# Optimization experiments

Hardware: AMD Instinct MI355X
Metric: run time of the kernel (lower is better)

Reference implementation:

```python
import jax, jax.numpy as jnp
import numpy as np

HID = 128
N_NODES = 50000
N_REL = 500
N_EDGES = 625000
BN_EPS = 1e-5
LRELU_SLOPE = 0.01


def _xavier(key, shape):
    fan_in, fan_out = shape[1], shape[0]
    std = float(np.sqrt(2.0 / (fan_in + fan_out)))
    return jax.random.normal(key, shape, dtype=jnp.float32) * std


def setup_inputs() -> dict:
    key = jax.random.key(0)
    ks = jax.random.split(key, 16)
    x = jax.random.normal(ks[0], (N_NODES, HID), dtype=jnp.float32)
    r = jax.random.normal(ks[1], (N_REL, HID), dtype=jnp.float32)
    que_context = jax.random.normal(ks[2], (1, HID), dtype=jnp.float32)
    fin_que = jax.random.normal(ks[3], (1, 1, HID), dtype=jnp.float32)
    edge_index = jax.random.randint(ks[4], (2, N_EDGES), 0, N_NODES, dtype=jnp.int64)
    edge_attr = jax.random.randint(ks[5], (N_EDGES,), 0, N_REL, dtype=jnp.int64)
    return {
        "x": x, "r": r, "que_context": que_context, "fin_que": fin_que,
        "edge_index": edge_index, "edge_attr": edge_attr,
        # mess_comp: Linear(2*hid, hid) + Tanh
        "W_mess": _xavier(ks[6], (HID, 2 * HID)), "b_mess": jnp.zeros((HID,), jnp.float32),
        # mess_atten_trans: Linear(2*hid, hid) + LeakyReLU
        "W_matt": _xavier(ks[7], (HID, 2 * HID)), "b_matt": jnp.zeros((HID,), jnp.float32),
        "mess_atten_weight": _xavier(ks[8], (1, HID)),
        # x_atten_trans: Linear(2*hid, hid) + LeakyReLU
        "W_xatt": _xavier(ks[9], (HID, 2 * HID)), "b_xatt": jnp.zeros((HID,), jnp.float32),
        "x_atten_weight": _xavier(ks[10], (1, HID)),
        # BatchNorm1d(hid) affine params (training-mode batch stats are used)
        "bn_gamma": jnp.ones((HID,), jnp.float32), "bn_beta": jnp.zeros((HID,), jnp.float32),
    }


def reference(x, r, que_context, fin_que, edge_index, edge_attr,
              W_mess, b_mess, W_matt, b_matt, mess_atten_weight,
              W_xatt, b_xatt, x_atten_weight, bn_gamma, bn_beta):
    n_nodes = x.shape[0]
    # BatchNorm1d over relation embeddings (training-mode: batch statistics, biased var)
    mu = jnp.mean(r, axis=0)
    var = jnp.mean(jnp.square(r - mu), axis=0)
    r = (r - mu) * jax.lax.rsqrt(var + BN_EPS) * bn_gamma + bn_beta

    head_ents, tail_ents = edge_index[0], edge_index[1]
    head_embeds = x[head_ents]            # [E, H]
    rel_embeds = r[edge_attr]             # [E, H]

    # message computation: Linear(2H->H) + tanh
    mess_in = jnp.concatenate([head_embeds, rel_embeds], axis=1)  # [E, 2H]
    mess = jnp.tanh(mess_in @ W_mess.T + b_mess)                  # [E, H]

    # message attention logits
    qc = jnp.broadcast_to(que_context, (mess.shape[0], que_context.shape[1]))
    mc = jnp.concatenate([mess, qc], axis=1) @ W_matt.T + b_matt
    mc = jax.nn.leaky_relu(mc, LRELU_SLOPE)
    mess_coeffs = jnp.sum(mess_atten_weight * mc, axis=1)         # [E]

    # segment softmax over tail_ents
    seg_max = jax.ops.segment_max(mess_coeffs, tail_ents, num_segments=n_nodes)
    mess_coeffs = jnp.exp(mess_coeffs - seg_max[tail_ents])
    seg_sum = jax.ops.segment_sum(mess_coeffs, tail_ents, num_segments=n_nodes)
    mess_weights = mess_coeffs / (seg_sum[tail_ents] + 1e-16)

    # weighted scatter-sum aggregation
    sum_mess = jax.ops.segment_sum(mess * mess_weights[:, None], tail_ents,
                                   num_segments=n_nodes)          # [N, H]

    # gating attention between x and aggregated messages
    pair = jnp.stack([x, sum_mess], axis=1)                       # [N, 2, H]
    fq = jnp.broadcast_to(fin_que, (n_nodes, 2, fin_que.shape[2]))
    xc = jnp.concatenate([pair, fq], axis=2)                      # [N, 2, 2H]
    xc = jax.nn.leaky_relu(jnp.einsum('nkc,hc->nkh', xc, W_xatt) + b_xatt, LRELU_SLOPE)
    x_coeffs = jnp.sum(x_atten_weight[None] * xc, axis=2)         # [N, 2]
    x_weight = jax.nn.softmax(x_coeffs, axis=1)
    x_out = x_weight[:, 0:1] * x + x_weight[:, 1:2] * sum_mess
    # dropout is identity (eval / p=0)
    return x_out, r
```

## Files before the change

kernel.cpp:

```cpp
#include <hip/hip_runtime.h>
#include <hip/hip_bf16.h>

#define HID 128
#define NN 50000
#define NR 500
#define NE 625000
#define LRELU 0.01f
#define SCAN_BLOCKS 196
#define NBLK_SC 256

typedef __hip_bfloat16 bf16;
typedef __attribute__((ext_vector_type(8))) short short8;
typedef __attribute__((ext_vector_type(4))) float float4_;

__device__ __forceinline__ float b2f(bf16 v) { return __bfloat162float(v); }
__device__ __forceinline__ bf16 f2b(float v) { return __float2bfloat16(v); }

__device__ __forceinline__ float san(float v) {
    return (v == v && v > -1e30f && v < 1e30f) ? v : 0.f;
}

__device__ __forceinline__ float ftanh(float a) {
    float e = __expf(2.f * a);
    return 1.f - 2.f * __builtin_amdgcn_rcpf(e + 1.f);
}

__device__ __forceinline__ float ldf(const void* p, int i, int f32) {
    return f32 ? ((const float*)p)[i] : b2f(((const bf16*)p)[i]);
}
__device__ __forceinline__ void stf(void* p, int i, float v, int f32) {
    if (f32) ((float*)p)[i] = v;
    else ((bf16*)p)[i] = f2b(v);
}

__device__ __forceinline__ int clampi(int v, int hi) {
    return v < 0 ? 0 : (v >= hi ? hi - 1 : v);
}
__device__ __forceinline__ int idx_at(const int* p, int i, int is64) {
    return p[is64 ? (2 * i) : i];
}

__device__ __forceinline__ unsigned short bfbits(float v) {
    bf16 h = f2b(v);
    return *(unsigned short*)&h;
}
__device__ __forceinline__ unsigned int packbf2(float a, float b) {
    return (unsigned int)bfbits(a) | ((unsigned int)bfbits(b) << 16);
}
__device__ __forceinline__ float bflo(unsigned int u) { return __uint_as_float(u << 16); }
__device__ __forceinline__ float bfhi(unsigned int u) { return __uint_as_float(u & 0xffff0000u); }

__device__ __forceinline__ float xorReduce16(float v) {
    v += __shfl_xor(v, 1, 64);
    v += __shfl_xor(v, 2, 64);
    v += __shfl_xor(v, 4, 64);
    v += __shfl_xor(v, 8, 64);
    return v;
}
__device__ __forceinline__ float waveMax(float v) {
#pragma unroll
    for (int o = 1; o < 64; o <<= 1) v = fmaxf(v, __shfl_xor(v, o, 64));
    return v;
}
__device__ __forceinline__ float waveSum(float v) {
#pragma unroll
    for (int o = 1; o < 64; o <<= 1) v += __shfl_xor(v, o, 64);
    return v;
}

__device__ __forceinline__ float dot8(const void* W, int row, int col, int f32,
                                      const float* vec) {
    float s;
    if (f32) {
        const float* p = (const float*)W + (size_t)row * 2 * HID + col;
        float4 a = *(const float4*)p;
        float4 b = *(const float4*)(p + 4);
        s = a.x * vec[0] + a.y * vec[1] + a.z * vec[2] + a.w * vec[3]
          + b.x * vec[4] + b.y * vec[5] + b.z * vec[6] + b.w * vec[7];
    } else {
        short8 v = *(const short8*)((const bf16*)W + (size_t)row * 2 * HID + col);
        s = 0.f;
#pragma unroll
        for (int i = 0; i < 8; ++i) {
            unsigned int u = ((unsigned int)(unsigned short)v[i]) << 16;
            s += __uint_as_float(u) * vec[i];
        }
    }
    return s;
}

__device__ __forceinline__ int octant_of(int head) {
    return (head * 8) / NN;
}

struct DetectArr {
    const void* p[16];
    int sz[16];
    int kind[16];
};

__global__ void detect_all(DetectArr d, int* __restrict__ flags) {
    int b = blockIdx.x;
    int t = threadIdx.x;
    if (d.kind[b] == 1) {
        if (t < 64) {
            const int* q = (const int*)d.p[b];
            int o = q[2 * t + 1];
            unsigned long long bm = __ballot(o != 0);
            if (t == 0) flags[b] = (bm == 0ull) ? 1 : 0;
        }
        return;
    }
    __shared__ int sb[256], sf[256];
    const unsigned int* w = (const unsigned int*)d.p[b];
    int K = d.sz[b] >> 1;
    if (K > 4096) K = 4096;
    int bv = 0, fv = 0;
    for (int i = t; i < K; i += 256) {
        unsigned int x = w[i];
        unsigned int lo = x & 0xFFFFu, hi = x >> 16;
        if (lo == 0u) {
            if (hi) fv++;
        } else {
            unsigned int e = (lo >> 7) & 0xFFu;
            if (e >= 90u && e <= 160u) bv++;
            else fv++;
        }
    }
    sb[t] = bv; sf[t] = fv;
    __syncthreads();
    for (int o = 128; o > 0; o >>= 1) {
        if (t < o) { sb[t] += sb[t + o]; sf[t] += sf[t + o]; }
        __syncthreads();
    }
    if (t == 0) flags[b] = (sf[0] > sb[0]) ? 1 : 0;
}

__global__ void bn_stats(const void* __restrict__ r, const int* __restrict__ flags,
                         float* __restrict__ stats) {
    __shared__ float sb[256], sq[256];
    const int fr = flags[1];
    int h = blockIdx.x;
    int t = threadIdx.x;
    float s = 0.f, ss = 0.f;
    for (int i = t; i < NR; i += 256) {
        float v = ldf(r, i * HID + h, fr);
        s += v; ss += v * v;
    }
    sb[t] = s; sq[t] = ss;
    __syncthreads();
    for (int o = 128; o > 0; o >>= 1) {
        if (t < o) { sb[t] += sb[t + o]; sq[t] += sq[t + o]; }
        __syncthreads();
    }
    if (t == 0) {
        float mu = sb[0] / NR;
        float var = sq[0] / NR - mu * mu;
        if (var < 0.f) var = 0.f;
        stats[h] = mu;
        stats[HID + h] = rsqrtf(var + 1e-5f);
    }
}

__global__ void bn_apply(const void* __restrict__ r, const void* __restrict__ gamma,
                         const void* __restrict__ beta, const int* __restrict__ flags,
                         const float* __restrict__ stats,
                         float* __restrict__ rnorm, void* __restrict__ out_base) {
    const int fr = flags[1], fg = flags[14], fb = flags[15], fo = flags[0];
    int i = blockIdx.x * 256 + threadIdx.x;
    if (i >= NR * HID) return;
    int h = i & 127;
    float v = san((ldf(r, i, fr) - stats[h]) * stats[HID + h] * ldf(gamma, h, fg)
                  + ldf(beta, h, fb));
    rnorm[i] = v;
    stf(out_base, NN * HID + i, v, fo);
}

__global__ void precomp_kernel(const void* __restrict__ Wmatt, const void* __restrict__ bmatt,
                               const void* __restrict__ qc,
                               const void* __restrict__ Wxatt, const void* __restrict__ bxatt,
                               const void* __restrict__ fq, const int* __restrict__ flags,
                               float* __restrict__ cmatt, float* __restrict__ cxatt) {
    __shared__ float vs[HID];
    __shared__ float part[256];
    const void* W    = blockIdx.x ? Wxatt : Wmatt;
    const void* bias = blockIdx.x ? bxatt : bmatt;
    const void* vsrc = blockIdx.x ? fq : qc;
    float* out       = blockIdx.x ? cxatt : cmatt;
    const int fW = flags[blockIdx.x ? 11 : 8];
    const int fb = flags[blockIdx.x ? 12 : 9];
    const int fv = flags[blockIdx.x ? 3 : 2];
    int t = threadIdx.x;
    if (t < HID) vs[t] = ldf(vsrc, t, fv);
    __syncthreads();
    int h = t & 127, ks = t >> 7;
    float a = 0.f;
#pragma unroll
    for (int i = 0; i < 8; ++i)
        a += dot8(W, h, HID + ks * 64 + i * 8, fW, &vs[ks * 64 + i * 8]);
    part[t] = a;
    __syncthreads();
    if (t < HID) out[h] = san(part[h] + part[h + 128] + ldf(bias, h, fb));
}

__global__ void rm_kernel(const void* __restrict__ Wmess, const void* __restrict__ bmess,
                          const int* __restrict__ flags,
                          const float* __restrict__ rnorm, bf16* __restrict__ Rmb) {
    __shared__ float rl[2][HID];
    const int fW = flags[6], fb = flags[7];
    int t = threadIdx.x;
    int sub = t >> 7, h = t & 127;
    int rel = blockIdx.x * 2 + sub;
    rl[sub][h] = rnorm[rel * HID + h];
    __syncthreads();
    float a = ldf(bmess, h, fb);
#pragma unroll
    for (int i = 0; i < 16; ++i)
        a += dot8(Wmess, h, HID + i * 8, fW, &rl[sub][i * 8]);
    Rmb[rel * HID + h] = f2b(san(a));
}

#define MLDA 136

__device__ __forceinline__ short8 load_bfrag(const void* W, int n, int k0, int f32) {
    short8 b;
    if (f32) {
        const float* Wf = (const float*)W + (size_t)n * 2 * HID + k0;
        float4 u0 = *(const float4*)Wf;
        float4 u1 = *(const float4*)(Wf + 4);
        b[0] = (short)bfbits(u0.x); b[1] = (short)bfbits(u0.y);
        b[2] = (short)bfbits(u0.z); b[3] = (short)bfbits(u0.w);
        b[4] = (short)bfbits(u1.x); b[5] = (short)bfbits(u1.y);
        b[6] = (short)bfbits(u1.z); b[7] = (short)bfbits(u1.w);
    } else {
        b = *(const short8*)((const bf16*)W + (size_t)n * 2 * HID + k0);
    }
    return b;
}

__global__ __launch_bounds__(256, 4) void xm_mfma(const void* __restrict__ x,
                                                  const void* __restrict__ Wmess,
                                                  const int* __restrict__ flags,
                                                  bf16* __restrict__ Xmb) {
    __shared__ short ml[64 * MLDA];
    const int fx = flags[0], fW = flags[6];
    int tid = threadIdx.x;
    int l = tid & 63, w = tid >> 6;
    int quad = l >> 4, lo16 = l & 15;
    int nbase = w * 32;
    short8 bfr[2][4];
#pragma unroll
    for (int nt = 0; nt < 2; ++nt)
#pragma unroll
        for (int kk = 0; kk < 4; ++kk)
            bfr[nt][kk] = load_bfrag(Wmess, nbase + nt * 16 + lo16, kk * 32 + quad * 8, fW);

    const int ntiles = (NN + 63) / 64;
    for (int tile = blockIdx.x; tile < ntiles; tile += gridDim.x) {
        __syncthreads();
#pragma unroll
        for (int p = 0; p < 8; ++p) {
            int rl_ = p * 8 + (tid >> 5);
            int node = clampi(tile * 64 + rl_, NN);
            int k4 = (tid & 31) * 4;
            unsigned int o0, o1;
            if (fx) {
                float4 v = *(const float4*)((const float*)x + (size_t)node * HID + k4);
                o0 = packbf2(v.x, v.y);
                o1 = packbf2(v.z, v.w);
            } else {
                uint2 u = *(const uint2*)((const bf16*)x + (size_t)node * HID + k4);
                o0 = u.x; o1 = u.y;
            }
            unsigned int* dst = (unsigned int*)&ml[rl_ * MLDA + k4];
            dst[0] = o0; dst[1] = o1;
        }
        __syncthreads();
        float4_ acc[4][2];
#pragma unroll
        for (int mt = 0; mt < 4; ++mt)
#pragma unroll
            for (int nt = 0; nt < 2; ++nt)
                acc[mt][nt] = (float4_){0.f, 0.f, 0.f, 0.f};
#pragma unroll
        for (int kk = 0; kk < 4; ++kk) {
            short8 a[4];
#pragma unroll
            for (int mt = 0; mt < 4; ++mt)
                a[mt] = *(const short8*)&ml[(mt * 16 + lo16) * MLDA + kk * 32 + quad * 8];
#pragma unroll
            for (int mt = 0; mt < 4; ++mt)
#pragma unroll
                for (int nt = 0; nt < 2; ++nt)
                    acc[mt][nt] = __builtin_amdgcn_mfma_f32_16x16x32_bf16(
                        a[mt], bfr[nt][kk], acc[mt][nt], 0, 0, 0);
        }
#pragma unroll
        for (int mt = 0; mt < 4; ++mt)
#pragma unroll
            for (int nt = 0; nt < 2; ++nt)
#pragma unroll
                for (int r = 0; r < 4; ++r) {
                    int node = tile * 64 + mt * 16 + quad * 4 + r;
                    if (node < NN)
                        Xmb[node * HID + nbase + nt * 16 + lo16] = f2b(san(acc[mt][nt][r]));
                }
    }
}

__global__ __launch_bounds__(256, 6) void edge_coeff_mfma(
        const bf16* __restrict__ Xmb, const bf16* __restrict__ Rmb,
        const void* __restrict__ Wmatt, const float* __restrict__ cmatt,
        const void* __restrict__ maw, const unsigned int* __restrict__ ohr,
        const int* __restrict__ oslot, const int* __restrict__ ooffs,
        const int* __restrict__ flags, float* __restrict__ ccsr,
        bf16* __restrict__ messT) {
    __shared__ short ml[64 * MLDA];
    __shared__ float swave[4][64];
    const int fWm = flags[8], fmw = flags[10];
    int tid = threadIdx.x;
    int l = tid & 63, w = tid >> 6;
    int quad = l >> 4, lo16 = l & 15;
    int nbase = w * 32;
    short8 bfr[2][4];
#pragma unroll
    for (int nt = 0; nt < 2; ++nt)
#pragma unroll
        for (int kk = 0; kk < 4; ++kk)
            bfr[nt][kk] = load_bfrag(Wmatt, nbase + nt * 16 + lo16, kk * 32 + quad * 8, fWm);

    int n0 = nbase + lo16, n1 = n0 + 16;
    float c0 = cmatt[n0], c1 = cmatt[n1];
    float w0 = ldf(maw, n0, fmw), w1 = ldf(maw, n1, fmw);

    const int k = blockIdx.x & 7;
    const int beg = ooffs[k], end = ooffs[k + 1];
    const int tstride = gridDim.x >> 3;
    const int seg = tid & 15;
    const int rowsub = tid >> 4;

    for (int t = blockIdx.x >> 3;; t += tstride) {
        int base = beg + t * 64;
        if (base >= end) break;
        __syncthreads();
        int rslot[4];
#pragma unroll
        for (int p = 0; p < 4; ++p) {
            int el = p * 16 + rowsub;
            int i = base + el;
            int idx = i < end ? i : end - 1;
            unsigned int hr = ohr[idx];
            rslot[p] = (i < end) ? oslot[i] : -1;
            int head = hr & 0xffffu, rel = hr >> 16;
            int k8 = seg * 8;
            uint4 xv = *(const uint4*)&Xmb[head * HID + k8];
            uint4 rv = *(const uint4*)&Rmb[rel * HID + k8];
            uint4 o;
            o.x = packbf2(ftanh(bflo(xv.x) + bflo(rv.x)), ftanh(bfhi(xv.x) + bfhi(rv.x)));
            o.y = packbf2(ftanh(bflo(xv.y) + bflo(rv.y)), ftanh(bfhi(xv.y) + bfhi(rv.y)));
            o.z = packbf2(ftanh(bflo(xv.z) + bflo(rv.z)), ftanh(bfhi(xv.z) + bfhi(rv.z)));
            o.w = packbf2(ftanh(bflo(xv.w) + bflo(rv.w)), ftanh(bfhi(xv.w) + bfhi(rv.w)));
            *(uint4*)&ml[el * MLDA + k8] = o;
        }
        __syncthreads();
        float4_ acc[4][2];
#pragma unroll
        for (int mt = 0; mt < 4; ++mt)
#pragma unroll
            for (int nt = 0; nt < 2; ++nt)
                acc[mt][nt] = (float4_){0.f, 0.f, 0.f, 0.f};
#pragma unroll
        for (int kk = 0; kk < 4; ++kk) {
            short8 a[4];
#pragma unroll
            for (int mt = 0; mt < 4; ++mt)
                a[mt] = *(const short8*)&ml[(mt * 16 + lo16) * MLDA + kk * 32 + quad * 8];
#pragma unroll
            for (int mt = 0; mt < 4; ++mt)
#pragma unroll
                for (int nt = 0; nt < 2; ++nt)
                    acc[mt][nt] = __builtin_amdgcn_mfma_f32_16x16x32_bf16(
                        a[mt], bfr[nt][kk], acc[mt][nt], 0, 0, 0);
        }
        if (messT) {
#pragma unroll
            for (int p = 0; p < 4; ++p) {
                int slot = rslot[p];
                if (slot >= 0) {
                    int el = p * 16 + rowsub;
                    *(uint4*)&messT[(size_t)slot * HID + seg * 8] =
                        *(const uint4*)&ml[el * MLDA + seg * 8];
                }
            }
        }
#pragma unroll
        for (int mt = 0; mt < 4; ++mt)
#pragma unroll
            for (int r = 0; r < 4; ++r) {
                float z0 = acc[mt][0][r] + c0;
                z0 = z0 > 0.f ? z0 : LRELU * z0;
                float z1 = acc[mt][1][r] + c1;
                z1 = z1 > 0.f ? z1 : LRELU * z1;
                float s = w0 * z0 + w1 * z1;
                s = xorReduce16(s);
                if (lo16 == 0) swave[w][mt * 16 + quad * 4 + r] = s;
            }
        __syncthreads();
        if (tid < 64) {
            int i = base + tid;
            if (i < end) {
                int slot = oslot[i];
                ccsr[slot] = san(swave[0][tid] + swave[1][tid]
                                 + swave[2][tid] + swave[3][tid]);
            }
        }
    }
}

__global__ __launch_bounds__(256, 4) void gate_mfma(
        const void* __restrict__ x, const bf16* __restrict__ smb,
        const void* __restrict__ Wxatt, const float* __restrict__ cxatt,
        const void* __restrict__ xaw, const int* __restrict__ flags,
        void* __restrict__ outx) {
    __shared__ short ml[64 * MLDA];
    __shared__ float swave[4][64];
    __shared__ float lgL[64];
    const int fx = flags[0], fWx = flags[11], fxw = flags[13], fo = flags[0];
    int tid = threadIdx.x;
    int l = tid & 63, w = tid >> 6;
    int quad = l >> 4, lo16 = l & 15;
    int nbase = w * 32;
    short8 bfr[2][4];
#pragma unroll
    for (int nt = 0; nt < 2; ++nt)
#pragma unroll
        for (int kk = 0; kk < 4; ++kk)
            bfr[nt][kk] = load_bfrag(Wxatt, nbase + nt * 16 + lo16, kk * 32 + quad * 8, fWx);

    int n0 = nbase + lo16, n1 = n0 + 16;
    float c0 = cxatt[n0], c1 = cxatt[n1];
    float w0 = ldf(xaw, n0, fxw), w1 = ldf(xaw, n1, fxw);

    const int ntiles = (NN + 31) / 32;
    for (int tile = blockIdx.x; tile < ntiles; tile += gridDim.x) {
        __syncthreads();
#pragma unroll
        for (int p = 0; p < 8; ++p) {
            int rl_ = p * 8 + (tid >> 5);
            int node = clampi(tile * 32 + (rl_ >> 1), NN);
            int k4 = (tid & 31) * 4;
            unsigned int o0, o1;
            if (rl_ & 1) {
                uint2 u = *(const uint2*)&smb[node * HID + k4];
                o0 = u.x; o1 = u.y;
            } else if (fx) {
                float4 v = *(const float4*)((const float*)x + (size_t)node * HID + k4);
                o0 = packbf2(v.x, v.y);
                o1 = packbf2(v.z, v.w);
            } else {
                uint2 u = *(const uint2*)((const bf16*)x + (size_t)node * HID + k4);
                o0 = u.x; o1 = u.y;
            }
            unsigned int* dst = (unsigned int*)&ml[rl_ * MLDA + k4];
            dst[0] = o0; dst[1] = o1;
        }
        __syncthreads();
        float4_ acc[4][2];
#pragma unroll
        for (int mt = 0; mt < 4; ++mt)
#pragma unroll
            for (int nt = 0; nt < 2; ++nt)
                acc[mt][nt] = (float4_){0.f, 0.f, 0.f, 0.f};
#pragma unroll
        for (int kk = 0; kk < 4; ++kk) {
            short8 a[4];
#pragma unroll
            for (int mt = 0; mt < 4; ++mt)
                a[mt] = *(const short8*)&ml[(mt * 16 + lo16) * MLDA + kk * 32 + quad * 8];
#pragma unroll
            for (int mt = 0; mt < 4; ++mt)
#pragma unroll
                for (int nt = 0; nt < 2; ++nt)
                    acc[mt][nt] = __builtin_amdgcn_mfma_f32_16x16x32_bf16(
                        a[mt], bfr[nt][kk], acc[mt][nt], 0, 0, 0);
        }
#pragma unroll
        for (int mt = 0; mt < 4; ++mt)
#pragma unroll
            for (int r = 0; r < 4; ++r) {
                float z0 = acc[mt][0][r] + c0;
                z0 = z0 > 0.f ? z0 : LRELU * z0;
                float z1 = acc[mt][1][r] + c1;
                z1 = z1 > 0.f ? z1 : LRELU * z1;
                float s = w0 * z0 + w1 * z1;
                s = xorReduce16(s);
                if (lo16 == 0) swave[w][mt * 16 + quad * 4 + r] = s;
            }
        __syncthreads();
        if (tid < 64)
            lgL[tid] = san(swave[0][tid] + swave[1][tid] + swave[2][tid] + swave[3][tid]);
        __syncthreads();
#pragma unroll
        for (int it = 0; it < 16; ++it) {
            int idx = tid + 256 * it;
            int nl = idx >> 7, h = idx & 127;
            int node = tile * 32 + nl;
            if (node < NN) {
                float g0 = lgL[2 * nl], g1 = lgL[2 * nl + 1];
                float mm = fmaxf(g0, g1);
                float e0 = __expf(g0 - mm), e1 = __expf(g1 - mm);
                float inv = __builtin_amdgcn_rcpf(e0 + e1);
                float xv = ldf(x, node * HID + h, fx);
                float sv = b2f(smb[node * HID + h]);
                stf(outx, node * HID + h, san((e0 * xv + e1 * sv) * inv), fo);
            }
        }
    }
}

__global__ void count_kernel(const int* __restrict__ ei, const int* __restrict__ flags,
                             int* __restrict__ counts, int* __restrict__ blockOct) {
    __shared__ int oh[8];
    const int is64e = flags[4];
    if (threadIdx.x < 8) oh[threadIdx.x] = 0;
    __syncthreads();
    for (int e = blockIdx.x * blockDim.x + threadIdx.x; e < NE; e += gridDim.x * blockDim.x) {
        int tail = clampi(idx_at(ei, NE + e, is64e), NN);
        int head = clampi(idx_at(ei, e, is64e), NN);
        atomicAdd(&counts[tail], 1);
        atomicAdd(&oh[octant_of(head)], 1);
    }
    __syncthreads();
    if (threadIdx.x < 8) blockOct[blockIdx.x * 8 + threadIdx.x] = oh[threadIdx.x];
}

__global__ void scan_phase1(const int* __restrict__ counts, int* __restrict__ offs,
                            int* __restrict__ bsum) {
    __shared__ int buf[256];
    int t = threadIdx.x;
    int i = blockIdx.x * 256 + t;
    int v = (i < NN) ? counts[i] : 0;
    buf[t] = v;
    __syncthreads();
    for (int off = 1; off < 256; off <<= 1) {
        int add = (t >= off) ? buf[t - off] : 0;
        __syncthreads();
        buf[t] += add;
        __syncthreads();
    }
    if (i < NN) offs[i] = buf[t] - v;
    if (t == 255) bsum[blockIdx.x] = buf[255];
}

__global__ void scan_phase2(int* __restrict__ bsum, int* __restrict__ bexc) {
    __shared__ int buf[256];
    int t = threadIdx.x;
    int v = (t < SCAN_BLOCKS) ? bsum[t] : 0;
    buf[t] = v;
    __syncthreads();
    for (int off = 1; off < 256; off <<= 1) {
        int add = (t >= off) ? buf[t - off] : 0;
        __syncthreads();
        buf[t] += add;
        __syncthreads();
    }
    if (t < SCAN_BLOCKS) bexc[t] = buf[t] - v;
    if (t == 255) bexc[SCAN_BLOCKS] = buf[255];
}

__global__ void scan_phase3(int* __restrict__ offs, int* __restrict__ cursor,
                            const int* __restrict__ bexc) {
    int i = blockIdx.x * 256 + threadIdx.x;
    if (i < NN) {
        int v = offs[i] + bexc[blockIdx.x];
        offs[i] = v;
        cursor[i] = v;
    }
    if (i == 0) offs[NN] = bexc[SCAN_BLOCKS];
}

__global__ void oct_scan(const int* __restrict__ blockOct, int* __restrict__ ooffs,
                         int* __restrict__ blockBase) {
    __shared__ int buf[256];
    __shared__ int excl[256][8];
    __shared__ int octTot[8], octBase[9];
    int t = threadIdx.x;
#pragma unroll
    for (int oo = 0; oo < 8; ++oo) {
        int v = blockOct[t * 8 + oo];
        buf[t] = v;
        __syncthreads();
        for (int off = 1; off < 256; off <<= 1) {
            int add = (t >= off) ? buf[t - off] : 0;
            __syncthreads();
            buf[t] += add;
            __syncthreads();
        }
        excl[t][oo] = buf[t] - v;
        if (t == 255) octTot[oo] = buf[255];
        __syncthreads();
    }
    if (t == 0) {
        int acc = 0;
        for (int oo = 0; oo < 8; ++oo) { octBase[oo] = acc; acc += octTot[oo]; }
        octBase[8] = acc;
        for (int i = 0; i < 9; ++i) ooffs[i] = octBase[i];
    }
    __syncthreads();
#pragma unroll
    for (int oo = 0; oo < 8; ++oo)
        blockBase[t * 8 + oo] = excl[t][oo] + octBase[oo];
}

__global__ void scatter_kernel(const int* __restrict__ ei, const int* __restrict__ ea,
                               const int* __restrict__ flags,
                               int* __restrict__ cursorT, const int* __restrict__ blockBase,
                               unsigned int* __restrict__ hrcsr,
                               unsigned int* __restrict__ ohr, int* __restrict__ oslot) {
    __shared__ int cur[8];
    const int is64e = flags[4], is64a = flags[5];
    if (threadIdx.x < 8) cur[threadIdx.x] = blockBase[blockIdx.x * 8 + threadIdx.x];
    __syncthreads();
    for (int e = blockIdx.x * blockDim.x + threadIdx.x; e < NE; e += gridDim.x * blockDim.x) {
        int tail = clampi(idx_at(ei, NE + e, is64e), NN);
        int head = clampi(idx_at(ei, e, is64e), NN);
        int rel = clampi(idx_at(ea, e, is64a), NR);
        unsigned int hr = (unsigned int)head | ((unsigned int)rel << 16);
        int p = atomicAdd(&cursorT[tail], 1);
        if (p >= 0 && p < NE) hrcsr[p] = hr;
        int q = atomicAdd(&cur[octant_of(head)], 1);
        if (q >= 0 && q < NE) {
            ohr[q] = hr;
            oslot[q] = (p >= 0 && p < NE) ? p : 0;
        }
    }
}

__global__ __launch_bounds__(256, 8) void node_aggr_seq(
        const bf16* __restrict__ messT, const int* __restrict__ offs,
        const float* __restrict__ ccsr, bf16* __restrict__ smb) {
    int tid = threadIdx.x;
    int sub = tid >> 6;
    int lane = tid & 63;
    int node = blockIdx.x * 4 + sub;
    if (node >= NN) return;
    int s = offs[node], en = offs[node + 1];

    float m = -INFINITY;
    for (int i = s + lane; i < en; i += 64) m = fmaxf(m, ccsr[i]);
    m = waveMax(m);
    float lsum = 0.f;
    for (int i = s + lane; i < en; i += 64) lsum += __expf(ccsr[i] - m);
    lsum = waveSum(lsum);
    float inv = 1.f / (lsum + 1e-16f);

    const int col = lane * 2;
    float acc0 = 0.f, acc1 = 0.f;
    int i = s;
    for (; i + 2 <= en; i += 2) {
        float wg0 = __expf(ccsr[i] - m), wg1 = __expf(ccsr[i + 1] - m);
        unsigned int u0 = *(const unsigned int*)&messT[(size_t)i * HID + col];
        unsigned int u1 = *(const unsigned int*)&messT[(size_t)(i + 1) * HID + col];
        acc0 += wg0 * bflo(u0) + wg1 * bflo(u1);
        acc1 += wg0 * bfhi(u0) + wg1 * bfhi(u1);
    }
    if (i < en) {
        float wg0 = __expf(ccsr[i] - m);
        unsigned int u0 = *(const unsigned int*)&messT[(size_t)i * HID + col];
        acc0 += wg0 * bflo(u0);
        acc1 += wg0 * bfhi(u0);
    }
    *(unsigned int*)&smb[node * HID + col] = packbf2(san(acc0 * inv), san(acc1 * inv));
}

__global__ __launch_bounds__(256, 8) void node_aggr_kernel(
        const bf16* __restrict__ Xmb, const bf16* __restrict__ Rmb,
        const int* __restrict__ offs, const unsigned int* __restrict__ hrcsr,
        const float* __restrict__ ccsr, bf16* __restrict__ smb) {
    int tid = threadIdx.x;
    int sub = tid >> 6;
    int lane = tid & 63;
    int node = blockIdx.x * 4 + sub;
    if (node >= NN) return;
    int s = offs[node], en = offs[node + 1];

    float m = -INFINITY;
    for (int i = s + lane; i < en; i += 64) m = fmaxf(m, ccsr[i]);
    m = waveMax(m);
    float lsum = 0.f;
    for (int i = s + lane; i < en; i += 64) lsum += __expf(ccsr[i] - m);
    lsum = waveSum(lsum);
    float inv = 1.f / (lsum + 1e-16f);

    const int col = lane * 2;
    float acc0 = 0.f, acc1 = 0.f;
    for (int i = s; i < en; ++i) {
        unsigned int hr0 = hrcsr[i];
        float wg0 = __expf(ccsr[i] - m);
        unsigned int xv0 = *(const unsigned int*)&Xmb[(hr0 & 0xffffu) * HID + col];
        unsigned int rv0 = *(const unsigned int*)&Rmb[(hr0 >> 16) * HID + col];
        acc0 += wg0 * ftanh(bflo(xv0) + bflo(rv0));
        acc1 += wg0 * ftanh(bfhi(xv0) + bfhi(rv0));
    }
    *(unsigned int*)&smb[node * HID + col] = packbf2(san(acc0 * inv), san(acc1 * inv));
}

extern "C" void kernel_launch(void* const* d_in, const int* in_sizes, int n_in,
                              void* d_out, int out_size, void* d_ws, size_t ws_size,
                              hipStream_t stream) {
    const void* x     = d_in[0];
    const void* r     = d_in[1];
    const void* qc    = d_in[2];
    const void* fq    = d_in[3];
    const int*  ei    = (const int*)d_in[4];
    const int*  ea    = (const int*)d_in[5];
    const void* Wmess = d_in[6];
    const void* bmess = d_in[7];
    const void* Wmatt = d_in[8];
    const void* bmatt = d_in[9];
    const void* maw   = d_in[10];
    const void* Wxatt = d_in[11];
    const void* bxatt = d_in[12];
    const void* xaw   = d_in[13];
    const void* gamma = d_in[14];
    const void* beta  = d_in[15];

    char* base = (char*)d_ws;
    size_t off = 0;
    auto alloc = [&](size_t bytes, size_t align) -> size_t {
        off = (off + align - 1) & ~(align - 1);
        size_t cur = off; off += bytes; return cur;
    };
    size_t o_flags  = alloc(16 * 4, 4);
    size_t o_counts = alloc((size_t)NN * 4, 4);
    size_t o_offs   = alloc((size_t)(NN + 1) * 4, 4);
    size_t o_cursor = alloc((size_t)(NN + 3) * 4, 4);
    size_t o_bsum   = alloc(256 * 4, 4);
    size_t o_bexc   = alloc(264 * 4, 4);
    size_t o_bOct   = alloc((size_t)NBLK_SC * 8 * 4, 4);
    size_t o_bBase  = alloc((size_t)NBLK_SC * 8 * 4, 4);
    size_t o_ooffs  = alloc(9 * 4, 4);
    size_t o_hrcsr  = alloc((size_t)NE * 4, 4);
    size_t o_ohr    = alloc((size_t)NE * 4, 4);
    size_t o_oslot  = alloc((size_t)NE * 4, 4);
    size_t o_ccsr   = alloc((size_t)NE * 4, 4);
    size_t o_rnorm  = alloc((size_t)NR * HID * 4, 4);
    size_t o_stats  = alloc(2 * HID * 4, 4);
    size_t o_cmatt  = alloc(HID * 4, 4);
    size_t o_cxatt  = alloc(HID * 4, 4);
    size_t o_Rmb    = alloc((size_t)NR * HID * 2, 4);
    size_t o_Xmb    = alloc((size_t)NN * HID * 2, 4);
    size_t o_smb    = alloc((size_t)NN * HID * 2, 4);
    size_t o_messT  = alloc((size_t)NE * HID * 2, 256);
    const bool useMess = ws_size >= off;

    int*          flags     = (int*)(base + o_flags);
    int*          counts    = (int*)(base + o_counts);
    int*          offs      = (int*)(base + o_offs);
    int*          cursor    = (int*)(base + o_cursor);
    int*          bsum      = (int*)(base + o_bsum);
    int*          bexc      = (int*)(base + o_bexc);
    int*          blockOct  = (int*)(base + o_bOct);
    int*          blockBase = (int*)(base + o_bBase);
    int*          ooffs     = (int*)(base + o_ooffs);
    unsigned int* hrcsr     = (unsigned int*)(base + o_hrcsr);
    unsigned int* ohr       = (unsigned int*)(base + o_ohr);
    int*          oslot     = (int*)(base + o_oslot);
    float*        ccsr      = (float*)(base + o_ccsr);
    float*        rnorm     = (float*)(base + o_rnorm);
    float*        stats     = (float*)(base + o_stats);
    float*        cmatt     = (float*)(base + o_cmatt);
    float*        cxatt     = (float*)(base + o_cxatt);
    bf16*         Rmb       = (bf16*)(base + o_Rmb);
    bf16*         Xmb       = (bf16*)(base + o_Xmb);
    bf16*         smb       = (bf16*)(base + o_smb);
    bf16*         messT     = useMess ? (bf16*)(base + o_messT) : (bf16*)nullptr;

    hipMemsetAsync(counts, 0, (size_t)NN * sizeof(int), stream);

    DetectArr da;
    const void* ps[16] = {x, r, qc, fq, ei, ea, Wmess, bmess, Wmatt, bmatt, maw,
                          Wxatt, bxatt, xaw, gamma, beta};
    int szs[16] = {NN * HID, NR * HID, HID, HID, 2 * NE, NE, 2 * HID * HID, HID,
                   2 * HID * HID, HID, HID, 2 * HID * HID, HID, HID, HID, HID};
    for (int i = 0; i < 16; ++i) {
        da.p[i] = ps[i];
        da.sz[i] = szs[i];
        da.kind[i] = (i == 4 || i == 5) ? 1 : 0;
    }
    detect_all<<<16, 256, 0, stream>>>(da, flags);

    bn_stats<<<HID, 256, 0, stream>>>(r, flags, stats);
    bn_apply<<<(NR * HID + 255) / 256, 256, 0, stream>>>(r, gamma, beta, flags, stats,
                                                         rnorm, d_out);
    precomp_kernel<<<2, 256, 0, stream>>>(Wmatt, bmatt, qc, Wxatt, bxatt, fq, flags,
                                          cmatt, cxatt);
    rm_kernel<<<NR / 2, 256, 0, stream>>>(Wmess, bmess, flags, rnorm, Rmb);
    xm_mfma<<<782, 256, 0, stream>>>(x, Wmess, flags, Xmb);
    count_kernel<<<NBLK_SC, 256, 0, stream>>>(ei, flags, counts, blockOct);
    scan_phase1<<<SCAN_BLOCKS, 256, 0, stream>>>(counts, offs, bsum);
    scan_phase2<<<1, 256, 0, stream>>>(bsum, bexc);
    scan_phase3<<<SCAN_BLOCKS, 256, 0, stream>>>(offs, cursor, bexc);
    oct_scan<<<1, 256, 0, stream>>>(blockOct, ooffs, blockBase);
    scatter_kernel<<<NBLK_SC, 256, 0, stream>>>(ei, ea, flags, cursor, blockBase,
                                                hrcsr, ohr, oslot);
    edge_coeff_mfma<<<1536, 256, 0, stream>>>(Xmb, Rmb, Wmatt, cmatt, maw, ohr, oslot,
                                              ooffs, flags, ccsr, messT);
    if (useMess)
        node_aggr_seq<<<(NN + 3) / 4, 256, 0, stream>>>(messT, offs, ccsr, smb);
    else
        node_aggr_kernel<<<(NN + 3) / 4, 256, 0, stream>>>(Xmb, Rmb, offs, hrcsr, ccsr,
                                                           smb);
    gate_mfma<<<1563, 256, 0, stream>>>(x, smb, Wxatt, cxatt, xaw, flags, d_out);
}
```

Baseline: 454.2 us.

## Drop materialized message buffer and recompute tanh messages during node aggregation

Removes the per-edge bf16 message buffer (E x 128) that edge_coeff_mfma scattered into CSR order, and always aggregates with node_aggr_kernel, which regathers the Xmb and Rmb rows and recomputes tanh per edge. The recompute loop in that kernel is also unrolled by two so more independent gathers are in flight. This avoids roughly 160 MB of global writes and reads for the message buffer. The cost is extra random gathers and repeated tanh work in the aggregation kernel.

```diff
diff --git a/kernel.cpp b/kernel.cpp
--- a/kernel.cpp
+++ b/kernel.cpp
@@ -313,8 +313,7 @@
         const void* __restrict__ Wmatt, const float* __restrict__ cmatt,
         const void* __restrict__ maw, const unsigned int* __restrict__ ohr,
         const int* __restrict__ oslot, const int* __restrict__ ooffs,
-        const int* __restrict__ flags, float* __restrict__ ccsr,
-        bf16* __restrict__ messT) {
+        const int* __restrict__ flags, float* __restrict__ ccsr) {
     __shared__ short ml[64 * MLDA];
     __shared__ float swave[4][64];
     const int fWm = flags[8], fmw = flags[10];
@@ -343,14 +342,12 @@
         int base = beg + t * 64;
         if (base >= end) break;
         __syncthreads();
-        int rslot[4];
 #pragma unroll
         for (int p = 0; p < 4; ++p) {
             int el = p * 16 + rowsub;
             int i = base + el;
             int idx = i < end ? i : end - 1;
             unsigned int hr = ohr[idx];
-            rslot[p] = (i < end) ? oslot[i] : -1;
             int head = hr & 0xffffu, rel = hr >> 16;
             int k8 = seg * 8;
             uint4 xv = *(const uint4*)&Xmb[head * HID + k8];
@@ -382,17 +379,6 @@
                     acc[mt][nt] = __builtin_amdgcn_mfma_f32_16x16x32_bf16(
                         a[mt], bfr[nt][kk], acc[mt][nt], 0, 0, 0);
         }
-        if (messT) {
-#pragma unroll
-            for (int p = 0; p < 4; ++p) {
-                int slot = rslot[p];
-                if (slot >= 0) {
-                    int el = p * 16 + rowsub;
-                    *(uint4*)&messT[(size_t)slot * HID + seg * 8] =
-                        *(const uint4*)&ml[el * MLDA + seg * 8];
-                }
-            }
-        }
 #pragma unroll
         for (int mt = 0; mt < 4; ++mt)
 #pragma unroll
@@ -408,11 +394,9 @@
         __syncthreads();
         if (tid < 64) {
             int i = base + tid;
-            if (i < end) {
-                int slot = oslot[i];
-                ccsr[slot] = san(swave[0][tid] + swave[1][tid]
-                                 + swave[2][tid] + swave[3][tid]);
-            }
+            if (i < end)
+                ccsr[oslot[i]] = san(swave[0][tid] + swave[1][tid]
+                                     + swave[2][tid] + swave[3][tid]);
         }
     }
 }
@@ -636,43 +620,6 @@
     }
 }
 
-__global__ __launch_bounds__(256, 8) void node_aggr_seq(
-        const bf16* __restrict__ messT, const int* __restrict__ offs,
-        const float* __restrict__ ccsr, bf16* __restrict__ smb) {
-    int tid = threadIdx.x;
-    int sub = tid >> 6;
-    int lane = tid & 63;
-    int node = blockIdx.x * 4 + sub;
-    if (node >= NN) return;
-    int s = offs[node], en = offs[node + 1];
-
-    float m = -INFINITY;
-    for (int i = s + lane; i < en; i += 64) m = fmaxf(m, ccsr[i]);
-    m = waveMax(m);
-    float lsum = 0.f;
-    for (int i = s + lane; i < en; i += 64) lsum += __expf(ccsr[i] - m);
-    lsum = waveSum(lsum);
-    float inv = 1.f / (lsum + 1e-16f);
-
-    const int col = lane * 2;
-    float acc0 = 0.f, acc1 = 0.f;
-    int i = s;
-    for (; i + 2 <= en; i += 2) {
-        float wg0 = __expf(ccsr[i] - m), wg1 = __expf(ccsr[i + 1] - m);
-        unsigned int u0 = *(const unsigned int*)&messT[(size_t)i * HID + col];
-        unsigned int u1 = *(const unsigned int*)&messT[(size_t)(i + 1) * HID + col];
-        acc0 += wg0 * bflo(u0) + wg1 * bflo(u1);
-        acc1 += wg0 * bfhi(u0) + wg1 * bfhi(u1);
-    }
-    if (i < en) {
-        float wg0 = __expf(ccsr[i] - m);
-        unsigned int u0 = *(const unsigned int*)&messT[(size_t)i * HID + col];
-        acc0 += wg0 * bflo(u0);
-        acc1 += wg0 * bfhi(u0);
-    }
-    *(unsigned int*)&smb[node * HID + col] = packbf2(san(acc0 * inv), san(acc1 * inv));
-}
-
 __global__ __launch_bounds__(256, 8) void node_aggr_kernel(
         const bf16* __restrict__ Xmb, const bf16* __restrict__ Rmb,
         const int* __restrict__ offs, const unsigned int* __restrict__ hrcsr,
@@ -694,7 +641,18 @@
 
     const int col = lane * 2;
     float acc0 = 0.f, acc1 = 0.f;
-    for (int i = s; i < en; ++i) {
+    int i = s;
+    for (; i + 2 <= en; i += 2) {
+        unsigned int hr0 = hrcsr[i], hr1 = hrcsr[i + 1];
+        float wg0 = __expf(ccsr[i] - m), wg1 = __expf(ccsr[i + 1] - m);
+        unsigned int xv0 = *(const unsigned int*)&Xmb[(hr0 & 0xffffu) * HID + col];
+        unsigned int rv0 = *(const unsigned int*)&Rmb[(hr0 >> 16) * HID + col];
+        unsigned int xv1 = *(const unsigned int*)&Xmb[(hr1 & 0xffffu) * HID + col];
+        unsigned int rv1 = *(const unsigned int*)&Rmb[(hr1 >> 16) * HID + col];
+        acc0 += wg0 * ftanh(bflo(xv0) + bflo(rv0)) + wg1 * ftanh(bflo(xv1) + bflo(rv1));
+        acc1 += wg0 * ftanh(bfhi(xv0) + bfhi(rv0)) + wg1 * ftanh(bfhi(xv1) + bfhi(rv1));
+    }
+    if (i < en) {
         unsigned int hr0 = hrcsr[i];
         float wg0 = __expf(ccsr[i] - m);
         unsigned int xv0 = *(const unsigned int*)&Xmb[(hr0 & 0xffffu) * HID + col];
@@ -751,8 +709,6 @@
     size_t o_Rmb    = alloc((size_t)NR * HID * 2, 4);
     size_t o_Xmb    = alloc((size_t)NN * HID * 2, 4);
     size_t o_smb    = alloc((size_t)NN * HID * 2, 4);
-    size_t o_messT  = alloc((size_t)NE * HID * 2, 256);
-    const bool useMess = ws_size >= off;
 
     int*          flags     = (int*)(base + o_flags);
     int*          counts    = (int*)(base + o_counts);
@@ -774,7 +730,6 @@
     bf16*         Rmb       = (bf16*)(base + o_Rmb);
     bf16*         Xmb       = (bf16*)(base + o_Xmb);
     bf16*         smb       = (bf16*)(base + o_smb);
-    bf16*         messT     = useMess ? (bf16*)(base + o_messT) : (bf16*)nullptr;
 
     hipMemsetAsync(counts, 0, (size_t)NN * sizeof(int), stream);
 
@@ -805,11 +760,7 @@
     scatter_kernel<<<NBLK_SC, 256, 0, stream>>>(ei, ea, flags, cursor, blockBase,
                                                 hrcsr, ohr, oslot);
     edge_coeff_mfma<<<1536, 256, 0, stream>>>(Xmb, Rmb, Wmatt, cmatt, maw, ohr, oslot,
-                                              ooffs, flags, ccsr, messT);
-    if (useMess)
-        node_aggr_seq<<<(NN + 3) / 4, 256, 0, stream>>>(messT, offs, ccsr, smb);
-    else
-        node_aggr_kernel<<<(NN + 3) / 4, 256, 0, stream>>>(Xmb, Rmb, offs, hrcsr, ccsr,
-                                                           smb);
+                                              ooffs, flags, ccsr);
+    node_aggr_kernel<<<(NN + 3) / 4, 256, 0, stream>>>(Xmb, Rmb, offs, hrcsr, ccsr, smb);
     gate_mfma<<<1563, 256, 0, stream>>>(x, smb, Wxatt, cxatt, xaw, flags, d_out);
 }
```

After: 411.8 us. 9.3% less time.
